# Kernel tuning notes

Measured on AMD Instinct MI355X. Metric: run time of the kernel, lower is better.

Reference implementation:

```python
import jax, jax.numpy as jnp
import numpy as np

B, E, N, F = 8, 2048, 2048, 128

def setup_inputs() -> dict:
    key = jax.random.key(0)
    k1, k2, k3, k4 = jax.random.split(key, 4)
    node_embeddings = jax.random.normal(k1, (B, N, F), dtype=jnp.float32)
    adj = jax.random.randint(k2, (B, E, N), -1, 3).astype(jnp.float32)
    W = jax.random.normal(k3, (F, F), dtype=jnp.float32) * (1.0 / np.sqrt(F))
    b = jax.random.normal(k4, (F,), dtype=jnp.float32) * 0.01
    return {"node_embeddings": node_embeddings, "adj": adj, "W": W, "b": b}

def reference(node_embeddings, adj, W, b):
    # adj_target: 1 where adj == -1, else 0
    adj_target = (adj == -1).astype(node_embeddings.dtype)          # [B, E, N]
    norm = jnp.sum(adj_target, axis=-1, keepdims=True)               # [B, E, 1]
    norm = jnp.where(norm == 0, 1.0, norm)
    # masked-mean aggregation of neighbor vertices into hyperedges
    message_vertex = jnp.matmul(adj_target, node_embeddings) / norm  # [B, E, F]
    # linear (torch Linear: x @ W.T + b) + relu
    hyperedge_embeddings = jax.nn.relu(jnp.matmul(message_vertex, W.T) + b)
    return hyperedge_embeddings
```

## Files before the change

kernel.cpp:

```cpp
#include <hip/hip_runtime.h>
#include <hip/hip_bf16.h>

#define B_ 8
#define E_ 2048
#define N_ 2048
#define F_ 128

#define BM 32
#define MT 2
#define BK 64
#define MP 136

using bf16x8 = __bf16 __attribute__((ext_vector_type(8)));
using fx4    = float __attribute__((ext_vector_type(4)));

__global__ __launch_bounds__(256) void prep_node(const float* __restrict__ node,
                                                 __bf16* __restrict__ nodeT) {
    const int bid = blockIdx.x;
    const int b   = bid & 7;
    const int n0  = (bid >> 3) * 32;
    const int t   = threadIdx.x;
    const int f   = t & 127;
    const int nb  = n0 + (t >> 7) * 16;

    const float* src = node + ((size_t)b * N_ + nb) * F_ + f;
    __bf16 h[16];
#pragma unroll
    for (int i = 0; i < 16; ++i)
        h[i] = (__bf16)src[(size_t)i * F_];

    __bf16* dst = nodeT + ((size_t)b * F_ + f) * N_ + nb;
    *(uint4*)&dst[0] = *(const uint4*)&h[0];
    *(uint4*)&dst[8] = *(const uint4*)&h[8];
}

__global__ __launch_bounds__(256, 2) void v2h_main(const float* __restrict__ adj,
                                                   const __bf16* __restrict__ nodeT,
                                                   const float* __restrict__ W,
                                                   const float* __restrict__ bias,
                                                   float* __restrict__ out) {
    __shared__ __align__(16) __bf16 Bs[2][128][64];
    __shared__ __align__(16) unsigned long long Abits[2][BM];
    __shared__ float normS[BM];
    __shared__ __align__(16) __bf16 Ms[BM * MP];

    const int t    = threadIdx.x;
    const int bid  = blockIdx.x;
    const int b    = bid & 7;
    const int e0   = (bid >> 3) * BM;
    const int w    = t >> 6;
    const int lane = t & 63;
    const int l15  = lane & 15;
    const int quad = lane >> 4;

    const int ar  = t >> 3;
    const int acs = t & 7;
    const float* aRow = adj + ((size_t)b * E_ + e0 + ar) * N_ + acs * 8;
    const __bf16* nTB = nodeT + (size_t)b * F_ * N_;

    auto issue_dma = [&](int k0, int buf) {
#pragma unroll
        for (int p = 0; p < 4; ++p) {
            int idx = t + 256 * p;
            int f   = idx >> 3;
            int sl  = idx & 7;
            int g   = sl ^ (f & 7);
            const __bf16* src = nTB + (size_t)f * N_ + k0 + g * 8;
            __bf16* dst = &Bs[buf][0][0] + (size_t)(w * 64 + 256 * p) * 8;
            __builtin_amdgcn_global_load_lds(
                (const __attribute__((address_space(1))) void*)src,
                (__attribute__((address_space(3))) void*)dst, 16, 0, 0);
        }
    };

    auto cvt8 = [](float4 v0, float4 v1) -> unsigned {
        unsigned m = 0;
        m |= (v0.x == -1.f) ? 1u   : 0u;
        m |= (v0.y == -1.f) ? 2u   : 0u;
        m |= (v0.z == -1.f) ? 4u   : 0u;
        m |= (v0.w == -1.f) ? 8u   : 0u;
        m |= (v1.x == -1.f) ? 16u  : 0u;
        m |= (v1.y == -1.f) ? 32u  : 0u;
        m |= (v1.z == -1.f) ? 64u  : 0u;
        m |= (v1.w == -1.f) ? 128u : 0u;
        return m;
    };

    auto unpack = [](unsigned byte) -> bf16x8 {
        union { unsigned u[4]; bf16x8 v; } r;
        r.u[0] = ((byte &   1u) ? 0x3F80u : 0u) | ((byte &   2u) ? 0x3F800000u : 0u);
        r.u[1] = ((byte &   4u) ? 0x3F80u : 0u) | ((byte &   8u) ? 0x3F800000u : 0u);
        r.u[2] = ((byte &  16u) ? 0x3F80u : 0u) | ((byte &  32u) ? 0x3F800000u : 0u);
        r.u[3] = ((byte &  64u) ? 0x3F80u : 0u) | ((byte & 128u) ? 0x3F800000u : 0u);
        return r.v;
    };

    fx4 acc[MT][2] = {};
    int cnt = 0;

    float4 a0 = *(const float4*)(aRow + 0);
    float4 a1 = *(const float4*)(aRow + 4);
    issue_dma(0, 0);
    {
        unsigned bits = cvt8(a0, a1);
        ((unsigned char*)&Abits[0][ar])[acs] = (unsigned char)bits;
        cnt += __popc(bits);
    }
    a0 = *(const float4*)(aRow + BK + 0);
    a1 = *(const float4*)(aRow + BK + 4);

#pragma unroll
    for (int m = 0; m < 32; ++m) {
        const int buf = m & 1;
        __syncthreads();

        if (m < 31) {
            issue_dma((m + 1) * BK, buf ^ 1);
            unsigned bits = cvt8(a0, a1);
            ((unsigned char*)&Abits[buf ^ 1][ar])[acs] = (unsigned char)bits;
            cnt += __popc(bits);
        }
        if (m < 30) {
            const float* ap = aRow + (m + 2) * BK;
            a0 = *(const float4*)(ap + 0);
            a1 = *(const float4*)(ap + 4);
        }

        bf16x8 af0[MT], af1[MT];
#pragma unroll
        for (int mt = 0; mt < MT; ++mt) {
            unsigned long long v = Abits[buf][mt * 16 + l15];
            unsigned lo = (unsigned)v, hi = (unsigned)(v >> 32);
            af0[mt] = unpack((lo >> (8 * quad)) & 255u);
            af1[mt] = unpack((hi >> (8 * quad)) & 255u);
        }

#pragma unroll
        for (int ft = 0; ft < 2; ++ft) {
            int f  = w * 32 + ft * 16 + l15;
            int q0 = quad ^ (f & 7);
            int q1 = (4 + quad) ^ (f & 7);
            bf16x8 b0 = *(const bf16x8*)&Bs[buf][f][q0 * 8];
#pragma unroll
            for (int mt = 0; mt < MT; ++mt)
                acc[mt][ft] = __builtin_amdgcn_mfma_f32_16x16x32_bf16(af0[mt], b0, acc[mt][ft], 0, 0, 0);
            bf16x8 b1 = *(const bf16x8*)&Bs[buf][f][q1 * 8];
#pragma unroll
            for (int mt = 0; mt < MT; ++mt)
                acc[mt][ft] = __builtin_amdgcn_mfma_f32_16x16x32_bf16(af1[mt], b1, acc[mt][ft], 0, 0, 0);
        }
    }

    {
        float c = (float)cnt;
        c += __shfl_xor(c, 1);
        c += __shfl_xor(c, 2);
        c += __shfl_xor(c, 4);
        if (acs == 0)
            normS[ar] = 1.f / fmaxf(c, 1.f);
    }
    __syncthreads();

    const int rbase = quad * 4;
    float4 rn[MT];
#pragma unroll
    for (int mt = 0; mt < MT; ++mt)
        rn[mt] = *(const float4*)&normS[mt * 16 + rbase];

#pragma unroll
    for (int ft = 0; ft < 2; ++ft) {
        int fcol = w * 32 + ft * 16 + l15;
#pragma unroll
        for (int mt = 0; mt < MT; ++mt) {
            const float* rr = (const float*)&rn[mt];
#pragma unroll
            for (int r = 0; r < 4; ++r)
                Ms[(mt * 16 + rbase + r) * MP + fcol] = (__bf16)(acc[mt][ft][r] * rr[r]);
        }
    }
    __syncthreads();

    fx4 acc2[MT][2] = {};
#pragma unroll
    for (int ks = 0; ks < 4; ++ks) {
        bf16x8 afm[MT];
#pragma unroll
        for (int mt = 0; mt < MT; ++mt)
            afm[mt] = *(const bf16x8*)&Ms[(mt * 16 + l15) * MP + ks * 32 + quad * 8];
#pragma unroll
        for (int gt = 0; gt < 2; ++gt) {
            int g = w * 32 + gt * 16 + l15;
            const float* wp = W + (size_t)g * F_ + ks * 32 + quad * 8;
            float4 wa = *(const float4*)wp;
            float4 wb = *(const float4*)(wp + 4);
            bf16x8 wfr;
            wfr[0] = (__bf16)wa.x; wfr[1] = (__bf16)wa.y;
            wfr[2] = (__bf16)wa.z; wfr[3] = (__bf16)wa.w;
            wfr[4] = (__bf16)wb.x; wfr[5] = (__bf16)wb.y;
            wfr[6] = (__bf16)wb.z; wfr[7] = (__bf16)wb.w;
#pragma unroll
            for (int mt = 0; mt < MT; ++mt)
                acc2[mt][gt] = __builtin_amdgcn_mfma_f32_16x16x32_bf16(afm[mt], wfr, acc2[mt][gt], 0, 0, 0);
        }
    }

#pragma unroll
    for (int gt = 0; gt < 2; ++gt) {
        int g = w * 32 + gt * 16 + l15;
        float bb = bias[g];
#pragma unroll
        for (int mt = 0; mt < MT; ++mt) {
#pragma unroll
            for (int r = 0; r < 4; ++r) {
                int e = e0 + mt * 16 + rbase + r;
                float v = acc2[mt][gt][r] + bb;
                out[((size_t)b * E_ + e) * F_ + g] = fmaxf(v, 0.f);
            }
        }
    }
}

extern "C" void kernel_launch(void* const* d_in, const int* in_sizes, int n_in,
                              void* d_out, int out_size, void* d_ws, size_t ws_size,
                              hipStream_t stream) {
    const float* node = (const float*)d_in[0];
    const float* adj  = (const float*)d_in[1];
    const float* W    = (const float*)d_in[2];
    const float* bias = (const float*)d_in[3];
    float* out = (float*)d_out;

    __bf16* nodeT = (__bf16*)d_ws;

    prep_node<<<512, 256, 0, stream>>>(node, nodeT);
    v2h_main<<<512, 256, 0, stream>>>(adj, nodeT, W, bias, out);
}
```

Baseline: 221.6 us.

## Fuse node transpose into cooperative kernel with larger tiles and bf16 W

```diff
diff --git a/kernel.cpp b/kernel.cpp
--- a/kernel.cpp
+++ b/kernel.cpp
@@ -1,70 +1,79 @@
 #include <hip/hip_runtime.h>
 #include <hip/hip_bf16.h>
+#include <hip/hip_cooperative_groups.h>
+
+namespace cg = cooperative_groups;
 
 #define B_ 8
 #define E_ 2048
 #define N_ 2048
 #define F_ 128
 
-#define BM 32
-#define MT 2
-#define BK 64
+#define BM 64
+#define MT 4
+#define BK 128
 #define MP 136
 
 using bf16x8 = __bf16 __attribute__((ext_vector_type(8)));
 using fx4    = float __attribute__((ext_vector_type(4)));
 
-__global__ __launch_bounds__(256) void prep_node(const float* __restrict__ node,
-                                                 __bf16* __restrict__ nodeT) {
-    const int bid = blockIdx.x;
-    const int b   = bid & 7;
-    const int n0  = (bid >> 3) * 32;
-    const int t   = threadIdx.x;
-    const int f   = t & 127;
-    const int nb  = n0 + (t >> 7) * 16;
-
-    const float* src = node + ((size_t)b * N_ + nb) * F_ + f;
-    __bf16 h[16];
-#pragma unroll
-    for (int i = 0; i < 16; ++i)
-        h[i] = (__bf16)src[(size_t)i * F_];
-
-    __bf16* dst = nodeT + ((size_t)b * F_ + f) * N_ + nb;
-    *(uint4*)&dst[0] = *(const uint4*)&h[0];
-    *(uint4*)&dst[8] = *(const uint4*)&h[8];
-}
-
-__global__ __launch_bounds__(256, 2) void v2h_main(const float* __restrict__ adj,
-                                                   const __bf16* __restrict__ nodeT,
+__global__ __launch_bounds__(256, 1) void v2h_coop(const float* __restrict__ node,
+                                                   const float* __restrict__ adj,
                                                    const float* __restrict__ W,
                                                    const float* __restrict__ bias,
+                                                   __bf16* __restrict__ nodeT,
+                                                   __bf16* __restrict__ Wb,
                                                    float* __restrict__ out) {
-    __shared__ __align__(16) __bf16 Bs[2][128][64];
-    __shared__ __align__(16) unsigned long long Abits[2][BM];
+    __shared__ __align__(16) __bf16 Bs[2][128][BK];
+    __shared__ __align__(16) unsigned Abits[2][BM][4];
     __shared__ float normS[BM];
     __shared__ __align__(16) __bf16 Ms[BM * MP];
 
     const int t    = threadIdx.x;
     const int bid  = blockIdx.x;
     const int b    = bid & 7;
-    const int e0   = (bid >> 3) * BM;
+    const int j    = bid >> 3;
+    const int e0   = j * BM;
     const int w    = t >> 6;
     const int lane = t & 63;
     const int l15  = lane & 15;
     const int quad = lane >> 4;
 
-    const int ar  = t >> 3;
-    const int acs = t & 7;
-    const float* aRow = adj + ((size_t)b * E_ + e0 + ar) * N_ + acs * 8;
+    {
+        const int f = t & 127;
+#pragma unroll
+        for (int u = 0; u < 2; ++u) {
+            const int nb = j * 64 + u * 32 + (t >> 7) * 16;
+            const float* src = node + ((size_t)b * N_ + nb) * F_ + f;
+            __bf16 h[16];
+#pragma unroll
+            for (int i = 0; i < 16; ++i)
+                h[i] = (__bf16)src[(size_t)i * F_];
+            __bf16* dst = nodeT + ((size_t)b * F_ + f) * N_ + nb;
+            *(uint4*)&dst[0] = *(const uint4*)&h[0];
+            *(uint4*)&dst[8] = *(const uint4*)&h[8];
+        }
+    }
+    if (bid < 16) {
+        int idx = bid * 256 + t;
+        float4 v = *(const float4*)&W[idx * 4];
+        __bf16 o[4] = {(__bf16)v.x, (__bf16)v.y, (__bf16)v.z, (__bf16)v.w};
+        *(uint2*)&Wb[idx * 4] = *(const uint2*)o;
+    }
+    cg::this_grid().sync();
+
+    const int ar  = t >> 2;
+    const int acs = t & 3;
+    const float* aRow = adj + ((size_t)b * E_ + e0 + ar) * N_ + acs * 32;
     const __bf16* nTB = nodeT + (size_t)b * F_ * N_;
 
     auto issue_dma = [&](int k0, int buf) {
 #pragma unroll
-        for (int p = 0; p < 4; ++p) {
+        for (int p = 0; p < 8; ++p) {
             int idx = t + 256 * p;
-            int f   = idx >> 3;
-            int sl  = idx & 7;
-            int g   = sl ^ (f & 7);
+            int f   = idx >> 4;
+            int sl  = idx & 15;
+            int g   = sl ^ (f & 15);
             const __bf16* src = nTB + (size_t)f * N_ + k0 + g * 8;
             __bf16* dst = &Bs[buf][0][0] + (size_t)(w * 64 + 256 * p) * 8;
             __builtin_amdgcn_global_load_lds(
@@ -73,16 +82,15 @@
         }
     };
 
-    auto cvt8 = [](float4 v0, float4 v1) -> unsigned {
+    auto cvt32 = [](const float4* a) -> unsigned {
         unsigned m = 0;
-        m |= (v0.x == -1.f) ? 1u   : 0u;
-        m |= (v0.y == -1.f) ? 2u   : 0u;
-        m |= (v0.z == -1.f) ? 4u   : 0u;
-        m |= (v0.w == -1.f) ? 8u   : 0u;
-        m |= (v1.x == -1.f) ? 16u  : 0u;
-        m |= (v1.y == -1.f) ? 32u  : 0u;
-        m |= (v1.z == -1.f) ? 64u  : 0u;
-        m |= (v1.w == -1.f) ? 128u : 0u;
+#pragma unroll
+        for (int i = 0; i < 8; ++i) {
+            m |= (a[i].x == -1.f) ? (1u << (4 * i))     : 0u;
+            m |= (a[i].y == -1.f) ? (1u << (4 * i + 1)) : 0u;
+            m |= (a[i].z == -1.f) ? (1u << (4 * i + 2)) : 0u;
+            m |= (a[i].w == -1.f) ? (1u << (4 * i + 3)) : 0u;
+        }
         return m;
     };
 
@@ -97,57 +105,61 @@
 
     fx4 acc[MT][2] = {};
     int cnt = 0;
-
-    float4 a0 = *(const float4*)(aRow + 0);
-    float4 a1 = *(const float4*)(aRow + 4);
+    float4 aR[8];
+
+#pragma unroll
+    for (int i = 0; i < 8; ++i) aR[i] = *(const float4*)(aRow + 4 * i);
     issue_dma(0, 0);
     {
-        unsigned bits = cvt8(a0, a1);
-        ((unsigned char*)&Abits[0][ar])[acs] = (unsigned char)bits;
+        unsigned bits = cvt32(aR);
+        Abits[0][ar][acs] = bits;
         cnt += __popc(bits);
     }
-    a0 = *(const float4*)(aRow + BK + 0);
-    a1 = *(const float4*)(aRow + BK + 4);
-
-#pragma unroll
-    for (int m = 0; m < 32; ++m) {
+#pragma unroll
+    for (int i = 0; i < 8; ++i) aR[i] = *(const float4*)(aRow + BK + 4 * i);
+
+#pragma unroll
+    for (int m = 0; m < 16; ++m) {
         const int buf = m & 1;
         __syncthreads();
 
-        if (m < 31) {
+        if (m < 15) {
             issue_dma((m + 1) * BK, buf ^ 1);
-            unsigned bits = cvt8(a0, a1);
-            ((unsigned char*)&Abits[buf ^ 1][ar])[acs] = (unsigned char)bits;
+            unsigned bits = cvt32(aR);
+            Abits[buf ^ 1][ar][acs] = bits;
             cnt += __popc(bits);
         }
-        if (m < 30) {
+        if (m < 14) {
             const float* ap = aRow + (m + 2) * BK;
-            a0 = *(const float4*)(ap + 0);
-            a1 = *(const float4*)(ap + 4);
-        }
-
-        bf16x8 af0[MT], af1[MT];
-#pragma unroll
-        for (int mt = 0; mt < MT; ++mt) {
-            unsigned long long v = Abits[buf][mt * 16 + l15];
-            unsigned lo = (unsigned)v, hi = (unsigned)(v >> 32);
-            af0[mt] = unpack((lo >> (8 * quad)) & 255u);
-            af1[mt] = unpack((hi >> (8 * quad)) & 255u);
-        }
-
-#pragma unroll
-        for (int ft = 0; ft < 2; ++ft) {
-            int f  = w * 32 + ft * 16 + l15;
-            int q0 = quad ^ (f & 7);
-            int q1 = (4 + quad) ^ (f & 7);
-            bf16x8 b0 = *(const bf16x8*)&Bs[buf][f][q0 * 8];
-#pragma unroll
-            for (int mt = 0; mt < MT; ++mt)
-                acc[mt][ft] = __builtin_amdgcn_mfma_f32_16x16x32_bf16(af0[mt], b0, acc[mt][ft], 0, 0, 0);
-            bf16x8 b1 = *(const bf16x8*)&Bs[buf][f][q1 * 8];
-#pragma unroll
-            for (int mt = 0; mt < MT; ++mt)
-                acc[mt][ft] = __builtin_amdgcn_mfma_f32_16x16x32_bf16(af1[mt], b1, acc[mt][ft], 0, 0, 0);
+#pragma unroll
+            for (int i = 0; i < 8; ++i) aR[i] = *(const float4*)(ap + 4 * i);
+        }
+
+        uint4 va[MT];
+#pragma unroll
+        for (int mt = 0; mt < MT; ++mt)
+            va[mt] = *(const uint4*)&Abits[buf][mt * 16 + l15][0];
+
+#pragma unroll
+        for (int s = 0; s < 4; ++s) {
+            bf16x8 af[MT];
+            const unsigned* vp0 = (const unsigned*)&va[0];
+            const unsigned* vp1 = (const unsigned*)&va[1];
+            const unsigned* vp2 = (const unsigned*)&va[2];
+            const unsigned* vp3 = (const unsigned*)&va[3];
+            af[0] = unpack((vp0[s] >> (8 * quad)) & 255u);
+            af[1] = unpack((vp1[s] >> (8 * quad)) & 255u);
+            af[2] = unpack((vp2[s] >> (8 * quad)) & 255u);
+            af[3] = unpack((vp3[s] >> (8 * quad)) & 255u);
+            const int slot = (s * 4 + quad) ^ l15;
+#pragma unroll
+            for (int ft = 0; ft < 2; ++ft) {
+                int f = w * 32 + ft * 16 + l15;
+                bf16x8 bf = *(const bf16x8*)&Bs[buf][f][slot * 8];
+#pragma unroll
+                for (int mt = 0; mt < MT; ++mt)
+                    acc[mt][ft] = __builtin_amdgcn_mfma_f32_16x16x32_bf16(af[mt], bf, acc[mt][ft], 0, 0, 0);
+            }
         }
     }
 
@@ -155,7 +167,6 @@
         float c = (float)cnt;
         c += __shfl_xor(c, 1);
         c += __shfl_xor(c, 2);
-        c += __shfl_xor(c, 4);
         if (acs == 0)
             normS[ar] = 1.f / fmaxf(c, 1.f);
     }
@@ -190,14 +201,7 @@
 #pragma unroll
         for (int gt = 0; gt < 2; ++gt) {
             int g = w * 32 + gt * 16 + l15;
-            const float* wp = W + (size_t)g * F_ + ks * 32 + quad * 8;
-            float4 wa = *(const float4*)wp;
-            float4 wb = *(const float4*)(wp + 4);
-            bf16x8 wfr;
-            wfr[0] = (__bf16)wa.x; wfr[1] = (__bf16)wa.y;
-            wfr[2] = (__bf16)wa.z; wfr[3] = (__bf16)wa.w;
-            wfr[4] = (__bf16)wb.x; wfr[5] = (__bf16)wb.y;
-            wfr[6] = (__bf16)wb.z; wfr[7] = (__bf16)wb.w;
+            bf16x8 wfr = *(const bf16x8*)&Wb[(size_t)g * F_ + ks * 32 + quad * 8];
 #pragma unroll
             for (int mt = 0; mt < MT; ++mt)
                 acc2[mt][gt] = __builtin_amdgcn_mfma_f32_16x16x32_bf16(afm[mt], wfr, acc2[mt][gt], 0, 0, 0);
@@ -230,7 +234,10 @@
     float* out = (float*)d_out;
 
     __bf16* nodeT = (__bf16*)d_ws;
-
-    prep_node<<<512, 256, 0, stream>>>(node, nodeT);
-    v2h_main<<<512, 256, 0, stream>>>(adj, nodeT, W, bias, out);
+    __bf16* Wb    = (__bf16*)((char*)d_ws + 8 * 1024 * 1024);
+
+    void* args[] = {(void*)&node, (void*)&adj, (void*)&W, (void*)&bias,
+                    (void*)&nodeT, (void*)&Wb, (void*)&out};
+    hipLaunchCooperativeKernel((const void*)v2h_coop, dim3(256), dim3(256),
+                               args, 0, stream);
 }
```

Result: slower. 267.8 us (+20.8%).

## Replace LDS-staged pipeline with direct register loads and 64-row tiles

Applied to the files above, without the earlier changes.

```diff
diff --git a/kernel.cpp b/kernel.cpp
--- a/kernel.cpp
+++ b/kernel.cpp
@@ -6,8 +6,8 @@
 #define N_ 2048
 #define F_ 128
 
-#define BM 32
-#define MT 2
+#define BM 64
+#define MT 4
 #define BK 64
 #define MP 136
 
@@ -34,13 +34,11 @@
     *(uint4*)&dst[8] = *(const uint4*)&h[8];
 }
 
-__global__ __launch_bounds__(256, 2) void v2h_main(const float* __restrict__ adj,
+__global__ __launch_bounds__(256, 1) void v2h_main(const float* __restrict__ adj,
                                                    const __bf16* __restrict__ nodeT,
                                                    const float* __restrict__ W,
                                                    const float* __restrict__ bias,
                                                    float* __restrict__ out) {
-    __shared__ __align__(16) __bf16 Bs[2][128][64];
-    __shared__ __align__(16) unsigned long long Abits[2][BM];
     __shared__ float normS[BM];
     __shared__ __align__(16) __bf16 Ms[BM * MP];
 
@@ -53,25 +51,15 @@
     const int l15  = lane & 15;
     const int quad = lane >> 4;
 
-    const int ar  = t >> 3;
-    const int acs = t & 7;
-    const float* aRow = adj + ((size_t)b * E_ + e0 + ar) * N_ + acs * 8;
-    const __bf16* nTB = nodeT + (size_t)b * F_ * N_;
-
-    auto issue_dma = [&](int k0, int buf) {
-#pragma unroll
-        for (int p = 0; p < 4; ++p) {
-            int idx = t + 256 * p;
-            int f   = idx >> 3;
-            int sl  = idx & 7;
-            int g   = sl ^ (f & 7);
-            const __bf16* src = nTB + (size_t)f * N_ + k0 + g * 8;
-            __bf16* dst = &Bs[buf][0][0] + (size_t)(w * 64 + 256 * p) * 8;
-            __builtin_amdgcn_global_load_lds(
-                (const __attribute__((address_space(1))) void*)src,
-                (__attribute__((address_space(3))) void*)dst, 16, 0, 0);
-        }
-    };
+    const float* aP[MT];
+#pragma unroll
+    for (int mt = 0; mt < MT; ++mt)
+        aP[mt] = adj + ((size_t)b * E_ + e0 + mt * 16 + l15) * N_ + quad * 8;
+    const __bf16* bP[2];
+#pragma unroll
+    for (int ft = 0; ft < 2; ++ft)
+        bP[ft] = nodeT + (size_t)b * F_ * N_
+               + (size_t)(w * 32 + ft * 16 + l15) * N_ + quad * 8;
 
     auto cvt8 = [](float4 v0, float4 v1) -> unsigned {
         unsigned m = 0;
@@ -85,7 +73,6 @@
         m |= (v1.w == -1.f) ? 128u : 0u;
         return m;
     };
-
     auto unpack = [](unsigned byte) -> bf16x8 {
         union { unsigned u[4]; bf16x8 v; } r;
         r.u[0] = ((byte &   1u) ? 0x3F80u : 0u) | ((byte &   2u) ? 0x3F800000u : 0u);
@@ -96,68 +83,74 @@
     };
 
     fx4 acc[MT][2] = {};
-    int cnt = 0;
-
-    float4 a0 = *(const float4*)(aRow + 0);
-    float4 a1 = *(const float4*)(aRow + 4);
-    issue_dma(0, 0);
-    {
-        unsigned bits = cvt8(a0, a1);
-        ((unsigned char*)&Abits[0][ar])[acs] = (unsigned char)bits;
-        cnt += __popc(bits);
-    }
-    a0 = *(const float4*)(aRow + BK + 0);
-    a1 = *(const float4*)(aRow + BK + 4);
+    int cnt[MT] = {};
+
+    float4 aR[MT][4];
+    uint4  bR[2][2];
+#pragma unroll
+    for (int mt = 0; mt < MT; ++mt) {
+        aR[mt][0] = *(const float4*)(aP[mt] + 0);
+        aR[mt][1] = *(const float4*)(aP[mt] + 4);
+        aR[mt][2] = *(const float4*)(aP[mt] + 32);
+        aR[mt][3] = *(const float4*)(aP[mt] + 36);
+    }
+#pragma unroll
+    for (int ft = 0; ft < 2; ++ft) {
+        bR[ft][0] = *(const uint4*)(bP[ft] + 0);
+        bR[ft][1] = *(const uint4*)(bP[ft] + 32);
+    }
 
 #pragma unroll
     for (int m = 0; m < 32; ++m) {
-        const int buf = m & 1;
-        __syncthreads();
+        bf16x8 af[MT][2];
+#pragma unroll
+        for (int mt = 0; mt < MT; ++mt) {
+            unsigned b0 = cvt8(aR[mt][0], aR[mt][1]);
+            unsigned b1 = cvt8(aR[mt][2], aR[mt][3]);
+            cnt[mt] += __popc(b0 | (b1 << 8));
+            af[mt][0] = unpack(b0);
+            af[mt][1] = unpack(b1);
+        }
+        bf16x8 bf[2][2];
+#pragma unroll
+        for (int ft = 0; ft < 2; ++ft) {
+            bf[ft][0] = *(const bf16x8*)&bR[ft][0];
+            bf[ft][1] = *(const bf16x8*)&bR[ft][1];
+        }
 
         if (m < 31) {
-            issue_dma((m + 1) * BK, buf ^ 1);
-            unsigned bits = cvt8(a0, a1);
-            ((unsigned char*)&Abits[buf ^ 1][ar])[acs] = (unsigned char)bits;
-            cnt += __popc(bits);
-        }
-        if (m < 30) {
-            const float* ap = aRow + (m + 2) * BK;
-            a0 = *(const float4*)(ap + 0);
-            a1 = *(const float4*)(ap + 4);
-        }
-
-        bf16x8 af0[MT], af1[MT];
-#pragma unroll
-        for (int mt = 0; mt < MT; ++mt) {
-            unsigned long long v = Abits[buf][mt * 16 + l15];
-            unsigned lo = (unsigned)v, hi = (unsigned)(v >> 32);
-            af0[mt] = unpack((lo >> (8 * quad)) & 255u);
-            af1[mt] = unpack((hi >> (8 * quad)) & 255u);
-        }
-
-#pragma unroll
-        for (int ft = 0; ft < 2; ++ft) {
-            int f  = w * 32 + ft * 16 + l15;
-            int q0 = quad ^ (f & 7);
-            int q1 = (4 + quad) ^ (f & 7);
-            bf16x8 b0 = *(const bf16x8*)&Bs[buf][f][q0 * 8];
-#pragma unroll
-            for (int mt = 0; mt < MT; ++mt)
-                acc[mt][ft] = __builtin_amdgcn_mfma_f32_16x16x32_bf16(af0[mt], b0, acc[mt][ft], 0, 0, 0);
-            bf16x8 b1 = *(const bf16x8*)&Bs[buf][f][q1 * 8];
-#pragma unroll
-            for (int mt = 0; mt < MT; ++mt)
-                acc[mt][ft] = __builtin_amdgcn_mfma_f32_16x16x32_bf16(af1[mt], b1, acc[mt][ft], 0, 0, 0);
-        }
-    }
-
-    {
-        float c = (float)cnt;
-        c += __shfl_xor(c, 1);
-        c += __shfl_xor(c, 2);
-        c += __shfl_xor(c, 4);
-        if (acs == 0)
-            normS[ar] = 1.f / fmaxf(c, 1.f);
+            const int ko = (m + 1) * BK;
+#pragma unroll
+            for (int mt = 0; mt < MT; ++mt) {
+                aR[mt][0] = *(const float4*)(aP[mt] + ko + 0);
+                aR[mt][1] = *(const float4*)(aP[mt] + ko + 4);
+                aR[mt][2] = *(const float4*)(aP[mt] + ko + 32);
+                aR[mt][3] = *(const float4*)(aP[mt] + ko + 36);
+            }
+#pragma unroll
+            for (int ft = 0; ft < 2; ++ft) {
+                bR[ft][0] = *(const uint4*)(bP[ft] + ko + 0);
+                bR[ft][1] = *(const uint4*)(bP[ft] + ko + 32);
+            }
+        }
+
+#pragma unroll
+        for (int kc = 0; kc < 2; ++kc)
+#pragma unroll
+            for (int ft = 0; ft < 2; ++ft)
+#pragma unroll
+                for (int mt = 0; mt < MT; ++mt)
+                    acc[mt][ft] = __builtin_amdgcn_mfma_f32_16x16x32_bf16(
+                        af[mt][kc], bf[ft][kc], acc[mt][ft], 0, 0, 0);
+    }
+
+#pragma unroll
+    for (int mt = 0; mt < MT; ++mt) {
+        float c = (float)cnt[mt];
+        c += __shfl_xor(c, 16);
+        c += __shfl_xor(c, 32);
+        if (w == 0 && quad == 0)
+            normS[mt * 16 + l15] = 1.f / fmaxf(c, 1.f);
     }
     __syncthreads();
 
@@ -200,7 +193,8 @@
             wfr[6] = (__bf16)wb.z; wfr[7] = (__bf16)wb.w;
 #pragma unroll
             for (int mt = 0; mt < MT; ++mt)
-                acc2[mt][gt] = __builtin_amdgcn_mfma_f32_16x16x32_bf16(afm[mt], wfr, acc2[mt][gt], 0, 0, 0);
+                acc2[mt][gt] = __builtin_amdgcn_mfma_f32_16x16x32_bf16(
+                    afm[mt], wfr, acc2[mt][gt], 0, 0, 0);
         }
     }
 
@@ -232,5 +226,5 @@
     __bf16* nodeT = (__bf16*)d_ws;
 
     prep_node<<<512, 256, 0, stream>>>(node, nodeT);
-    v2h_main<<<512, 256, 0, stream>>>(adj, nodeT, W, bias, out);
+    v2h_main<<<256, 256, 0, stream>>>(adj, nodeT, W, bias, out);
 }
```

Result: slower. 286.6 us (+29.3%).
